# Optimization experiments

Measured on AMD Instinct MI355X. Metric: run time of the kernel, lower is better.

## Reference

```python
import jax, jax.numpy as jnp
import numpy as np

B, N, E, H = 4, 2048, 256, 4
D = E // H  # dim_head = 64


def setup_inputs() -> dict:
    key = jax.random.key(0)
    ks = jax.random.split(key, 8)
    r = lambda k, shape, s=0.02: jax.random.normal(k, shape, jnp.float32) * s
    return dict(
        x0=jax.random.normal(ks[0], (B, N, E), jnp.float32),
        x1=jax.random.normal(ks[1], (B, N, E), jnp.float32),
        Wqk=r(ks[2], (E, E)), bqk=jnp.zeros((E,), jnp.float32),
        Wv=r(ks[3], (E, E)), bv=jnp.zeros((E,), jnp.float32),
        Wo=r(ks[4], (E, E)), bo=jnp.zeros((E,), jnp.float32),
        W1=r(ks[5], (2 * E, 2 * E)), b1=jnp.zeros((2 * E,), jnp.float32),
        g_ln=jnp.ones((2 * E,), jnp.float32), b_ln=jnp.zeros((2 * E,), jnp.float32),
        W2=r(ks[6], (E, 2 * E)), b2=jnp.zeros((E,), jnp.float32),
    )


def _ln(x, g, b, eps=1e-5):
    m = x.mean(-1, keepdims=True)
    v = x.var(-1, keepdims=True)
    return (x - m) * jax.lax.rsqrt(v + eps) * g + b


def reference(x0, x1, Wqk, bqk, Wv, bv, Wo, bo, W1, b1, g_ln, b_ln, W2, b2):
    lin = lambda x, W, b: x @ W.T + b  # torch Linear convention: W is [out, in]
    split = lambda t: t.reshape(B, N, H, D).transpose(0, 2, 1, 3)  # [B,H,N,D]
    merge = lambda t: t.transpose(0, 2, 1, 3).reshape(B, N, E)
    mult = D ** -0.25  # scale**0.5 applied to both qk0 and qk1

    qk0 = split(lin(x0, Wqk, bqk)) * mult
    qk1 = split(lin(x1, Wqk, bqk)) * mult
    v0 = split(lin(x0, Wv, bv))
    v1 = split(lin(x1, Wv, bv))

    sim = jnp.einsum('bhid,bhjd->bhij', qk0, qk1)  # shared similarity [B,H,N0,N1]
    attn01 = jax.nn.softmax(sim, axis=-1)                       # softmax over N1
    attn10 = jax.nn.softmax(jnp.swapaxes(sim, -2, -1), axis=-1)  # [B,H,N1,N0], softmax over N0

    m0 = jnp.einsum('bhij,bhjd->bhid', attn01, v1)  # messages to x0 tokens
    m1 = jnp.einsum('bhij,bhjd->bhid', attn10, v0)  # messages to x1 tokens
    m0 = lin(merge(m0), Wo, bo)
    m1 = lin(merge(m1), Wo, bo)

    def ffn(x, m):
        h = lin(jnp.concatenate([x, m], -1), W1, b1)
        h = jax.nn.gelu(_ln(h, g_ln, b_ln), approximate=False)  # torch GELU = exact erf
        return x + lin(h, W2, b2)

    return (ffn(x0, m0), ffn(x1, m1), attn01, attn10)
```

## Files before the change

kernel.cpp:

```cpp
#include <hip/hip_runtime.h>


typedef unsigned short u16;
typedef unsigned int u32;
typedef __bf16 bf16x8 __attribute__((ext_vector_type(8)));
typedef float f32x4 __attribute__((ext_vector_type(4)));

#define DEV static __device__ __forceinline__

constexpr float MULT2_ = 0.42466090013685146f;

DEV u16 f2bf(float f){ __bf16 h = (__bf16)f; return __builtin_bit_cast(u16, h); }
DEV float bf2f(u16 h){ return __builtin_bit_cast(float, (u32)h << 16); }

DEV f32x4 mfma16(bf16x8 a, bf16x8 b, f32x4 c){
  return __builtin_amdgcn_mfma_f32_16x16x32_bf16(a, b, c, 0, 0, 0);
}

DEV void barrier_ndv(){
  asm volatile("s_waitcnt lgkmcnt(0)" ::: "memory");
  __builtin_amdgcn_s_barrier();
  asm volatile("" ::: "memory");
}

typedef const __attribute__((address_space(1))) void cvoid_g;
typedef __attribute__((address_space(3))) void void_l;
DEV void gload16(const void* g, void* l){
  __builtin_amdgcn_global_load_lds((cvoid_g*)g, (void_l*)l, 16, 0, 0);
}

__global__ __launch_bounds__(256) void cast_k(
    const float* __restrict__ x0, const float* __restrict__ x1,
    const float* __restrict__ Wqk, const float* __restrict__ Wv,
    const float* __restrict__ Wo,  const float* __restrict__ W1,
    const float* __restrict__ W2,
    u16* __restrict__ xc0, u16* __restrict__ xc1,
    u16* __restrict__ Wqkv, u16* __restrict__ WoB,
    u16* __restrict__ W1B,  u16* __restrict__ W2B)
{
  int bid = blockIdx.x;
  if (bid < 1024){
    int s = bid >> 9;
    const float* x = s ? x1 : x0;
    u16* xc = s ? xc1 : xc0;
    for (int v = (bid&511)*256 + threadIdx.x; v < 8192*64; v += 512*256){
      float4 f = ((const float4*)x)[v];
      int m = v >> 6, e4 = (v & 63) << 2;
      ushort4 o;
      o.x = f2bf(f.x); o.y = f2bf(f.y); o.z = f2bf(f.z); o.w = f2bf(f.w);
      *(ushort4*)&xc[(size_t)m*512 + e4] = o;
    }
  } else {
    int t0 = (bid-1024)*256 + threadIdx.x;
    for (int t = t0; t < 512*256; t += 256*256)
      Wqkv[t] = f2bf(t < 65536 ? Wqk[t] : Wv[t - 65536]);
    for (int t = t0; t < 256*256; t += 256*256) WoB[t] = f2bf(Wo[t]);
    for (int t = t0; t < 512*512; t += 256*256) W1B[t] = f2bf(W1[t]);
    for (int t = t0; t < 256*512; t += 256*256) W2B[t] = f2bf(W2[t]);
  }
}

template<int EPI, int K, int LDA, int NT>
__global__ __launch_bounds__(256) void gemm_k(
    const u16* __restrict__ A0, const u16* __restrict__ A1,
    const u16* __restrict__ Bw,
    const float* __restrict__ bias, const float* __restrict__ bias2,
    u16* __restrict__ O0, u16* __restrict__ O1,
    u16* __restrict__ P0, u16* __restrict__ P1,
    const float* __restrict__ R0, const float* __restrict__ R1,
    float* __restrict__ Y)
{
  constexpr int MF = (NT==128) ? 4 : 2;
  __shared__ u16 As[2][128*32];
  __shared__ u16 Bs[2][NT*32];
  const int tid = threadIdx.x, w = tid>>6, l = tid&63;
  const int s = blockIdx.z;
  const u16* A = s ? A1 : A0;
  const int m0 = blockIdx.x*128, n0 = blockIdx.y*NT;
  const int wr = (NT==128) ? (w>>1)*64 : w*32;
  const int wc = (NT==128) ? (w&1)*64 : 0;
  const f32x4 z4 = {0.f,0.f,0.f,0.f};
  f32x4 acc[MF][4];
  #pragma unroll
  for (int i=0;i<MF;++i)
    #pragma unroll
    for (int j=0;j<4;++j) acc[i][j] = z4;
  const int srow = l>>2, sc8 = (l&3)*8;
  auto STAGE = [&](int buf, int kt){
    gload16(&A [(size_t)(m0+w*32   +srow)*LDA + kt + sc8], &As[buf][w*1024]);
    gload16(&A [(size_t)(m0+w*32+16+srow)*LDA + kt + sc8], &As[buf][w*1024+512]);
    if constexpr (NT==128){
      gload16(&Bw[(size_t)(n0+w*32   +srow)*K + kt + sc8], &Bs[buf][w*1024]);
      gload16(&Bw[(size_t)(n0+w*32+16+srow)*K + kt + sc8], &Bs[buf][w*1024+512]);
    } else {
      gload16(&Bw[(size_t)(n0+w*16+srow)*K + kt + sc8], &Bs[buf][w*512]);
    }
  };
  STAGE(0, 0);
  __syncthreads();
  int cur = 0;
  for (int kt = 0; kt < K; kt += 32){
    if (kt+32 < K) STAGE(cur^1, kt+32);
    bf16x8 af[MF], bfr[4];
    #pragma unroll
    for (int mf=0; mf<MF; ++mf)
      af[mf] = *(const bf16x8*)&As[cur][(wr+mf*16+(l&15))*32 + (l>>4)*8];
    #pragma unroll
    for (int nf=0; nf<4; ++nf)
      bfr[nf] = *(const bf16x8*)&Bs[cur][(wc+nf*16+(l&15))*32 + (l>>4)*8];
    #pragma unroll
    for (int mf=0; mf<MF; ++mf)
      #pragma unroll
      for (int nf=0; nf<4; ++nf)
        acc[mf][nf] = mfma16(af[mf], bfr[nf], acc[mf][nf]);
    __syncthreads();
    cur ^= 1;
  }
  u16* Oq = s ? O1 : O0;
  u16* Ov = s ? P1 : P0;
  const float* R = s ? R1 : R0;
  #pragma unroll
  for (int mf=0; mf<MF; ++mf){
    #pragma unroll
    for (int nf=0; nf<4; ++nf){
      #pragma unroll
      for (int r=0; r<4; ++r){
        int row = m0 + wr + mf*16 + (l>>4)*4 + r;
        int col = n0 + wc + nf*16 + (l&15);
        float v = acc[mf][nf][r];
        if constexpr (EPI==0){
          int bb = row >> 11, n = row & 2047;
          if (col < 256){
            float q = (v + bias[col]) * MULT2_;
            int hh = col >> 6, d = col & 63;
            Oq[(size_t)((bb*4+hh)*2048 + n)*64 + d] = f2bf(q);
          } else {
            int c2 = col - 256;
            int hh = c2 >> 6, d = c2 & 63;
            Ov[(size_t)((bb*4+hh)*2048 + n)*64 + d] = f2bf(v + bias2[c2]);
          }
        } else if constexpr (EPI==1){
          Oq[(size_t)row*512 + 256 + col] = f2bf(v + bias[col]);
        } else if constexpr (EPI==2){
          Oq[(size_t)row*512 + col] = f2bf(v + bias[col]);
        } else {
          float* Yp = Y + (size_t)s*2097152;
          Yp[(size_t)row*256 + col] = v + bias[col] + R[(size_t)row*256 + col];
        }
      }
    }
  }
}

__global__ __launch_bounds__(256) void transp_k(
    const u16* __restrict__ v0, const u16* __restrict__ v1,
    u16* __restrict__ t0p, u16* __restrict__ t1p)
{
  __shared__ u16 t[64*66];
  const u16* vin = blockIdx.z ? v1 : v0;
  u16* vout = blockIdx.z ? t1p : t0p;
  int bh = blockIdx.y, j0 = blockIdx.x*64, tid = threadIdx.x;
  #pragma unroll
  for (int r=0;r<2;++r){
    int j = r*32 + (tid>>3), d = (tid&7)*8;
    *(uint4*)&t[j*66 + d] = *(const uint4*)&vin[((size_t)bh*2048 + j0 + j)*64 + d];
  }
  __syncthreads();
  #pragma unroll
  for (int r=0;r<2;++r){
    int d = r*32 + (tid>>3), j8 = (tid&7)*8;
    u32 p[4];
    #pragma unroll
    for (int k=0;k<4;++k){
      u32 lo = t[(j8+2*k)*66 + d];
      u32 hi = t[(j8+2*k+1)*66 + d];
      p[k] = lo | (hi<<16);
    }
    uint4 o = {p[0],p[1],p[2],p[3]};
    *(uint4*)&vout[((size_t)bh*64 + d)*2048 + j0 + j8] = o;
  }
}

__global__ __launch_bounds__(256) void stats2_k(
    const u16* __restrict__ qk0, const u16* __restrict__ qk1,
    float* __restrict__ rps, float* __restrict__ psum)
{
  __shared__ u16 Ks[128*72];
  __shared__ float csumw[4*128];
  int bsw = (int)blockIdx.x;
  int id = (bsw&7)*128 + (bsw>>3);
  const int it = id & 15, jc = (id>>4)&3, bh = id>>6;
  const int i0 = it*128, j0 = jc*512;
  const int tid = threadIdx.x, w = tid>>6, l = tid&63;
  const u16* Qb = qk0 + (size_t)bh*2048*64;
  const u16* Kb = qk1 + (size_t)bh*2048*64;
  bf16x8 qf[2][2];
  #pragma unroll
  for (int mf=0; mf<2; ++mf)
    #pragma unroll
    for (int kf=0; kf<2; ++kf)
      qf[mf][kf] = *(const bf16x8*)&Qb[(size_t)(i0 + w*32 + mf*16 + (l&15))*64 + kf*32 + (l>>4)*8];
  float rlv[2][4];
  #pragma unroll
  for (int mf=0;mf<2;++mf)
    #pragma unroll
    for (int r=0;r<4;++r) rlv[mf][r] = 0.f;
  const int krow = tid>>3, kc = (tid&7)*8;
  uint4 kreg[4];
  #pragma unroll
  for (int r=0;r<4;++r)
    kreg[r] = *(const uint4*)&Kb[(size_t)(j0+r*32+krow)*64 + kc];
  const f32x4 z4 = {0.f,0.f,0.f,0.f};
  for (int jt=j0; jt<j0+512; jt+=128){
    barrier_ndv();
    #pragma unroll
    for (int r=0;r<4;++r) *(uint4*)&Ks[(r*32+krow)*72 + kc] = kreg[r];
    if (jt+128 < j0+512){
      #pragma unroll
      for (int r=0;r<4;++r)
        kreg[r] = *(const uint4*)&Kb[(size_t)(jt+128+r*32+krow)*64 + kc];
    }
    barrier_ndv();
    f32x4 acc[2][8];
    #pragma unroll
    for (int mf=0;mf<2;++mf)
      #pragma unroll
      for (int nf=0;nf<8;++nf) acc[mf][nf] = z4;
    #pragma unroll
    for (int nf=0; nf<8; ++nf){
      bf16x8 b0 = *(const bf16x8*)&Ks[(nf*16+(l&15))*72 + (l>>4)*8];
      bf16x8 b1 = *(const bf16x8*)&Ks[(nf*16+(l&15))*72 + 32 + (l>>4)*8];
      acc[0][nf] = mfma16(qf[0][0], b0, acc[0][nf]);
      acc[0][nf] = mfma16(qf[0][1], b1, acc[0][nf]);
      acc[1][nf] = mfma16(qf[1][0], b0, acc[1][nf]);
      acc[1][nf] = mfma16(qf[1][1], b1, acc[1][nf]);
    }
    #pragma unroll
    for (int mf=0;mf<2;++mf)
      #pragma unroll
      for (int nf=0;nf<8;++nf)
        #pragma unroll
        for (int r=0;r<4;++r)
          acc[mf][nf][r] = exp2f(acc[mf][nf][r]);
    #pragma unroll
    for (int mf=0; mf<2; ++mf)
      #pragma unroll
      for (int r=0; r<4; ++r){
        float ps = 0.f;
        #pragma unroll
        for (int nf=0; nf<8; ++nf) ps += acc[mf][nf][r];
        ps += __shfl_xor(ps, 1);
        ps += __shfl_xor(ps, 2);
        ps += __shfl_xor(ps, 4);
        ps += __shfl_xor(ps, 8);
        rlv[mf][r] += ps;
      }
    float cs[8];
    #pragma unroll
    for (int nf=0; nf<8; ++nf){
      float s = 0.f;
      #pragma unroll
      for (int mf=0;mf<2;++mf)
        #pragma unroll
        for (int r=0;r<4;++r) s += acc[mf][nf][r];
      s += __shfl_xor(s, 16);
      s += __shfl_xor(s, 32);
      cs[nf] = s;
    }
    if (l < 16){
      #pragma unroll
      for (int nf=0; nf<8; ++nf)
        csumw[w*128 + nf*16 + l] = cs[nf];
    }
    barrier_ndv();
    if (tid < 128){
      float s = csumw[tid] + csumw[128+tid] + csumw[256+tid] + csumw[384+tid];
      psum[((size_t)bh*16 + it)*2048 + jt + tid] = s;
    }
  }
  if ((l&15)==0){
    #pragma unroll
    for (int mf=0;mf<2;++mf)
      #pragma unroll
      for (int r=0;r<4;++r){
        int i = i0 + w*32 + mf*16 + (l>>4)*4 + r;
        rps[((size_t)bh*4 + jc)*2048 + i] = rlv[mf][r];
      }
  }
}

__global__ __launch_bounds__(256) void reduce_k(
    const float* __restrict__ rps, const float* __restrict__ psum,
    float* __restrict__ c0, float* __restrict__ c1)
{
  int idx = blockIdx.x*256 + threadIdx.x;
  int bh = idx >> 11, i = idx & 2047;
  if (blockIdx.y == 0){
    float s = 0.f;
    #pragma unroll
    for (int c=0;c<4;++c) s += rps[((size_t)bh*4 + c)*2048 + i];
    c0[bh*2048 + i] = log2f(s);
  } else {
    float s = 0.f;
    #pragma unroll
    for (int it=0; it<16; ++it) s += psum[((size_t)bh*16 + it)*2048 + i];
    c1[bh*2048 + i] = log2f(s);
  }
}

__global__ __launch_bounds__(256) void attn_k(
    const u16* __restrict__ qk0, const u16* __restrict__ qk1,
    const u16* __restrict__ vT0, const u16* __restrict__ vT1,
    const float* __restrict__ c0, const float* __restrict__ c1,
    u16* __restrict__ mo0, u16* __restrict__ mo1,
    float* __restrict__ dout)
{
  __shared__ u16 Ks[128*72];
  __shared__ u16 Vs[64*136];
  __shared__ u16 Ps[128*136];
  int bsw = (int)blockIdx.x;
  int id = (bsw&7)*64 + (bsw>>3);
  const int it = id & 15, bh = (id>>4)&15, z = id>>8;
  const u16* Q  = z ? qk1 : qk0;
  const u16* Kp = z ? qk0 : qk1;
  const u16* Vp = z ? vT0 : vT1;
  const float* cc = z ? c1 : c0;
  u16* mo = z ? mo1 : mo0;
  const int i0 = it*128;
  float* aout = dout + (size_t)(z ? 71303168u : 4194304u) + (size_t)bh*4194304u;
  const int tid = threadIdx.x, w = tid>>6, l = tid&63;
  const u16* Qb = Q + (size_t)bh*2048*64;
  const u16* Kb = Kp + (size_t)bh*2048*64;
  const u16* Vb = Vp + (size_t)bh*64*2048;
  bf16x8 qf[8][2];
  #pragma unroll
  for (int nf=0; nf<8; ++nf)
    #pragma unroll
    for (int kf=0; kf<2; ++kf)
      qf[nf][kf] = *(const bf16x8*)&Qb[(size_t)(i0 + nf*16 + (l&15))*64 + kf*32 + (l>>4)*8];
  float rci[8];
  #pragma unroll
  for (int nf=0;nf<8;++nf)
    rci[nf] = cc[bh*2048 + i0 + nf*16 + (l&15)];
  const f32x4 z4 = {0.f,0.f,0.f,0.f};
  f32x4 macc[2][4];
  #pragma unroll
  for (int mf=0;mf<2;++mf)
    #pragma unroll
    for (int nf=0;nf<4;++nf) macc[mf][nf] = z4;
  const int krow = tid>>3, kc = (tid&7)*8;
  const int vd = tid>>4, vc = (tid&15)*8;
  uint4 kreg[4], vreg[4];
  #pragma unroll
  for (int r=0;r<4;++r){
    kreg[r] = *(const uint4*)&Kb[(size_t)(r*32+krow)*64 + kc];
    vreg[r] = *(const uint4*)&Vb[(size_t)(r*16+vd)*2048 + vc];
  }
  for (int jt=0; jt<2048; jt+=128){
    barrier_ndv();
    #pragma unroll
    for (int r=0;r<4;++r) *(uint4*)&Ks[(r*32+krow)*72 + kc] = kreg[r];
    #pragma unroll
    for (int r=0;r<4;++r) *(uint4*)&Vs[(r*16+vd)*136 + vc] = vreg[r];
    if (jt+128 < 2048){
      #pragma unroll
      for (int r=0;r<4;++r){
        kreg[r] = *(const uint4*)&Kb[(size_t)(jt+128+r*32+krow)*64 + kc];
        vreg[r] = *(const uint4*)&Vb[(size_t)(r*16+vd)*2048 + jt+128 + vc];
      }
    }
    barrier_ndv();
    f32x4 acc[2][8];
    #pragma unroll
    for (int mf=0;mf<2;++mf)
      #pragma unroll
      for (int nf=0;nf<8;++nf) acc[mf][nf] = z4;
    #pragma unroll
    for (int mf=0; mf<2; ++mf){
      bf16x8 a0 = *(const bf16x8*)&Ks[(w*32+mf*16+(l&15))*72 + (l>>4)*8];
      bf16x8 a1 = *(const bf16x8*)&Ks[(w*32+mf*16+(l&15))*72 + 32 + (l>>4)*8];
      #pragma unroll
      for (int nf=0; nf<8; ++nf){
        acc[mf][nf] = mfma16(a0, qf[nf][0], acc[mf][nf]);
        acc[mf][nf] = mfma16(a1, qf[nf][1], acc[mf][nf]);
      }
    }
    #pragma unroll
    for (int mf=0;mf<2;++mf){
      int jlb = w*32 + mf*16 + (l>>4)*4;
      #pragma unroll
      for (int nf=0;nf<8;++nf){
        int i = nf*16 + (l&15);
        f32x4 pv;
        #pragma unroll
        for (int r=0;r<4;++r) pv[r] = exp2f(acc[mf][nf][r]-rci[nf]);
        __builtin_nontemporal_store(pv,
            (f32x4*)&aout[(size_t)(i0+i)*2048 + jt + jlb]);
        u16 pb[4];
        #pragma unroll
        for (int r=0;r<4;++r) pb[r] = f2bf(pv[r]);
        u32 w0 = (u32)pb[0] | ((u32)pb[1]<<16);
        u32 w1 = (u32)pb[2] | ((u32)pb[3]<<16);
        uint2 pk = {w0, w1};
        *(uint2*)&Ps[i*136 + jlb] = pk;
      }
    }
    barrier_ndv();
    #pragma unroll
    for (int kf=0; kf<4; ++kf){
      bf16x8 pa0 = *(const bf16x8*)&Ps[(w*32 + (l&15))*136 + kf*32 + (l>>4)*8];
      bf16x8 pa1 = *(const bf16x8*)&Ps[(w*32 + 16 + (l&15))*136 + kf*32 + (l>>4)*8];
      #pragma unroll
      for (int nf=0; nf<4; ++nf){
        bf16x8 vb = *(const bf16x8*)&Vs[(nf*16+(l&15))*136 + kf*32 + (l>>4)*8];
        macc[0][nf] = mfma16(pa0, vb, macc[0][nf]);
        macc[1][nf] = mfma16(pa1, vb, macc[1][nf]);
      }
    }
  }
  int bb = bh>>2, hh = bh&3;
  #pragma unroll
  for (int mf=0;mf<2;++mf)
    #pragma unroll
    for (int nf=0;nf<4;++nf)
      #pragma unroll
      for (int r=0;r<4;++r){
        int n = i0 + w*32 + mf*16 + (l>>4)*4 + r;
        int d = nf*16 + (l&15);
        mo[(size_t)(bb*2048 + n)*256 + hh*64 + d] = f2bf(macc[mf][nf][r]);
      }
}

__global__ __launch_bounds__(256) void ln_gelu_k(
    u16* __restrict__ h0, u16* __restrict__ h1,
    const float* __restrict__ g, const float* __restrict__ be)
{
  u16* h = blockIdx.y ? h1 : h0;
  int row = blockIdx.x*4 + (threadIdx.x>>6);
  int l = threadIdx.x & 63;
  u16* hr = h + (size_t)row*512;
  uint4 raw = *(const uint4*)&hr[l*8];
  u32 ua[4] = {raw.x, raw.y, raw.z, raw.w};
  float f[8];
  #pragma unroll
  for (int k=0;k<4;++k){
    f[2*k]   = bf2f((u16)(ua[k] & 0xFFFFu));
    f[2*k+1] = bf2f((u16)(ua[k] >> 16));
  }
  float s = 0.f, s2 = 0.f;
  #pragma unroll
  for (int k=0;k<8;++k){ s += f[k]; s2 += f[k]*f[k]; }
  #pragma unroll
  for (int o=1;o<64;o<<=1){ s += __shfl_xor(s,o); s2 += __shfl_xor(s2,o); }
  float mean = s * (1.f/512.f);
  float var  = s2 * (1.f/512.f) - mean*mean;
  float rstd = rsqrtf(var + 1e-5f);
  u32 ob[4];
  #pragma unroll
  for (int k=0;k<8;++k){
    int e = l*8 + k;
    float t = (f[k]-mean)*rstd*g[e] + be[e];
    float gl = 0.5f*t*(1.f + erff(t*0.70710678118654752f));
    u16 b = f2bf(gl);
    if (k&1) ob[k>>1] |= (u32)b << 16; else ob[k>>1] = (u32)b;
  }
  uint4 o4 = {ob[0],ob[1],ob[2],ob[3]};
  *(uint4*)&hr[l*8] = o4;
}

extern "C" void kernel_launch(void* const* d_in, const int* in_sizes, int n_in,
                              void* d_out, int out_size, void* d_ws, size_t ws_size,
                              hipStream_t stream)
{
  const float* x0  = (const float*)d_in[0];
  const float* x1  = (const float*)d_in[1];
  const float* Wqk = (const float*)d_in[2];
  const float* bqk = (const float*)d_in[3];
  const float* Wv  = (const float*)d_in[4];
  const float* bv  = (const float*)d_in[5];
  const float* Wo  = (const float*)d_in[6];
  const float* bo  = (const float*)d_in[7];
  const float* W1  = (const float*)d_in[8];
  const float* b1  = (const float*)d_in[9];
  const float* gln = (const float*)d_in[10];
  const float* bln = (const float*)d_in[11];
  const float* W2  = (const float*)d_in[12];
  const float* b2  = (const float*)d_in[13];
  (void)in_sizes; (void)n_in; (void)out_size; (void)ws_size;
  float* out = (float*)d_out;
  char* ws = (char*)d_ws;
  size_t off = 0;
  auto alloc = [&](size_t bytes)->void*{
    void* p = ws + off; off += (bytes + 255) & ~(size_t)255; return p; };
  u16* xc0 = (u16*)alloc((size_t)8192*512*2);
  u16* xc1 = (u16*)alloc((size_t)8192*512*2);
  u16* Wqkv= (u16*)alloc((size_t)512*256*2);
  u16* WoB = (u16*)alloc((size_t)256*256*2);
  u16* W1B = (u16*)alloc((size_t)512*512*2);
  u16* W2B = (u16*)alloc((size_t)256*512*2);
  u16* qk0 = (u16*)alloc((size_t)16*2048*64*2);
  u16* qk1 = (u16*)alloc((size_t)16*2048*64*2);
  u16* v0  = (u16*)alloc((size_t)16*2048*64*2);
  u16* v1  = (u16*)alloc((size_t)16*2048*64*2);
  u16* vT0 = (u16*)alloc((size_t)16*2048*64*2);
  u16* vT1 = (u16*)alloc((size_t)16*2048*64*2);
  u16* m0  = (u16*)alloc((size_t)8192*256*2);
  u16* m1  = (u16*)alloc((size_t)8192*256*2);
  u16* h0  = (u16*)alloc((size_t)8192*512*2);
  u16* h1  = (u16*)alloc((size_t)8192*512*2);
  float* c0 = (float*)alloc((size_t)16*2048*4);
  float* c1 = (float*)alloc((size_t)16*2048*4);
  float* psum = (float*)alloc((size_t)16*16*2048*4);
  float* rps  = (float*)alloc((size_t)16*4*2048*4);

  cast_k<<<dim3(1280), 256, 0, stream>>>(x0, x1, Wqk, Wv, Wo, W1, W2,
      xc0, xc1, Wqkv, WoB, W1B, W2B);
  gemm_k<0,256,512,128><<<dim3(64,4,2), 256, 0, stream>>>(
      xc0, xc1, Wqkv, bqk, bv, qk0, qk1, v0, v1, nullptr, nullptr, nullptr);
  transp_k<<<dim3(32,16,2), 256, 0, stream>>>(v0, v1, vT0, vT1);
  stats2_k<<<dim3(1024), 256, 0, stream>>>(qk0, qk1, rps, psum);
  reduce_k<<<dim3(128,2), 256, 0, stream>>>(rps, psum, c0, c1);
  attn_k<<<dim3(512), 256, 0, stream>>>(
      qk0, qk1, vT0, vT1, c0, c1, m0, m1, out);
  gemm_k<1,256,256,64><<<dim3(64,4,2), 256, 0, stream>>>(
      m0, m1, WoB, bo, nullptr, xc0, xc1, nullptr, nullptr, nullptr, nullptr, nullptr);
  gemm_k<2,512,512,128><<<dim3(64,4,2), 256, 0, stream>>>(
      xc0, xc1, W1B, b1, nullptr, h0, h1, nullptr, nullptr, nullptr, nullptr, nullptr);
  ln_gelu_k<<<dim3(2048,2), 256, 0, stream>>>(h0, h1, gln, bln);
  gemm_k<3,512,512,64><<<dim3(64,4,2), 256, 0, stream>>>(
      h0, h1, W2B, b2, nullptr, nullptr, nullptr, nullptr, nullptr, x0, x1, out);
}
```

Measured before the change: 313.3 us.

## Halve attention query tile, load K fragments directly to registers, raise occupancy

```diff
diff --git a/kernel.cpp b/kernel.cpp
--- a/kernel.cpp
+++ b/kernel.cpp
@@ -308,88 +308,88 @@
   }
 }
 
-__global__ __launch_bounds__(256) void attn_k(
+__global__ __launch_bounds__(256, 3) void attn_k(
     const u16* __restrict__ qk0, const u16* __restrict__ qk1,
     const u16* __restrict__ vT0, const u16* __restrict__ vT1,
     const float* __restrict__ c0, const float* __restrict__ c1,
     u16* __restrict__ mo0, u16* __restrict__ mo1,
     float* __restrict__ dout)
 {
-  __shared__ u16 Ks[128*72];
   __shared__ u16 Vs[64*136];
-  __shared__ u16 Ps[128*136];
+  __shared__ u16 Ps[64*136];
   int bsw = (int)blockIdx.x;
-  int id = (bsw&7)*64 + (bsw>>3);
-  const int it = id & 15, bh = (id>>4)&15, z = id>>8;
+  int id = (bsw&7)*128 + (bsw>>3);
+  const int it = id & 31, bh = (id>>5)&15, z = id>>9;
   const u16* Q  = z ? qk1 : qk0;
   const u16* Kp = z ? qk0 : qk1;
   const u16* Vp = z ? vT0 : vT1;
   const float* cc = z ? c1 : c0;
   u16* mo = z ? mo1 : mo0;
-  const int i0 = it*128;
+  const int i0 = it*64;
   float* aout = dout + (size_t)(z ? 71303168u : 4194304u) + (size_t)bh*4194304u;
   const int tid = threadIdx.x, w = tid>>6, l = tid&63;
   const u16* Qb = Q + (size_t)bh*2048*64;
   const u16* Kb = Kp + (size_t)bh*2048*64;
   const u16* Vb = Vp + (size_t)bh*64*2048;
-  bf16x8 qf[8][2];
-  #pragma unroll
-  for (int nf=0; nf<8; ++nf)
+  bf16x8 qf[4][2];
+  #pragma unroll
+  for (int nf=0; nf<4; ++nf)
     #pragma unroll
     for (int kf=0; kf<2; ++kf)
       qf[nf][kf] = *(const bf16x8*)&Qb[(size_t)(i0 + nf*16 + (l&15))*64 + kf*32 + (l>>4)*8];
-  float rci[8];
-  #pragma unroll
-  for (int nf=0;nf<8;++nf)
+  float rci[4];
+  #pragma unroll
+  for (int nf=0;nf<4;++nf)
     rci[nf] = cc[bh*2048 + i0 + nf*16 + (l&15)];
   const f32x4 z4 = {0.f,0.f,0.f,0.f};
-  f32x4 macc[2][4];
+  f32x4 macc[4];
+  #pragma unroll
+  for (int nf=0;nf<4;++nf) macc[nf] = z4;
+  const int kr0 = w*32 + (l&15);
+  bf16x8 ka[2][2], kaN[2][2];
   #pragma unroll
   for (int mf=0;mf<2;++mf)
     #pragma unroll
-    for (int nf=0;nf<4;++nf) macc[mf][nf] = z4;
-  const int krow = tid>>3, kc = (tid&7)*8;
+    for (int h=0;h<2;++h)
+      ka[mf][h] = *(const bf16x8*)&Kb[(size_t)(kr0 + mf*16)*64 + h*32 + (l>>4)*8];
   const int vd = tid>>4, vc = (tid&15)*8;
-  uint4 kreg[4], vreg[4];
-  #pragma unroll
-  for (int r=0;r<4;++r){
-    kreg[r] = *(const uint4*)&Kb[(size_t)(r*32+krow)*64 + kc];
+  uint4 vreg[4];
+  #pragma unroll
+  for (int r=0;r<4;++r)
     vreg[r] = *(const uint4*)&Vb[(size_t)(r*16+vd)*2048 + vc];
-  }
   for (int jt=0; jt<2048; jt+=128){
+    f32x4 acc[2][4];
+    #pragma unroll
+    for (int mf=0;mf<2;++mf)
+      #pragma unroll
+      for (int nf=0;nf<4;++nf) acc[mf][nf] = z4;
+    #pragma unroll
+    for (int mf=0; mf<2; ++mf)
+      #pragma unroll
+      for (int nf=0; nf<4; ++nf){
+        acc[mf][nf] = mfma16(ka[mf][0], qf[nf][0], acc[mf][nf]);
+        acc[mf][nf] = mfma16(ka[mf][1], qf[nf][1], acc[mf][nf]);
+      }
+    if (jt+128 < 2048){
+      #pragma unroll
+      for (int mf=0;mf<2;++mf)
+        #pragma unroll
+        for (int h=0;h<2;++h)
+          kaN[mf][h] = *(const bf16x8*)&Kb[(size_t)(jt+128 + kr0 + mf*16)*64 + h*32 + (l>>4)*8];
+    }
     barrier_ndv();
-    #pragma unroll
-    for (int r=0;r<4;++r) *(uint4*)&Ks[(r*32+krow)*72 + kc] = kreg[r];
     #pragma unroll
     for (int r=0;r<4;++r) *(uint4*)&Vs[(r*16+vd)*136 + vc] = vreg[r];
     if (jt+128 < 2048){
       #pragma unroll
-      for (int r=0;r<4;++r){
-        kreg[r] = *(const uint4*)&Kb[(size_t)(jt+128+r*32+krow)*64 + kc];
+      for (int r=0;r<4;++r)
         vreg[r] = *(const uint4*)&Vb[(size_t)(r*16+vd)*2048 + jt+128 + vc];
-      }
-    }
-    barrier_ndv();
-    f32x4 acc[2][8];
-    #pragma unroll
-    for (int mf=0;mf<2;++mf)
-      #pragma unroll
-      for (int nf=0;nf<8;++nf) acc[mf][nf] = z4;
-    #pragma unroll
-    for (int mf=0; mf<2; ++mf){
-      bf16x8 a0 = *(const bf16x8*)&Ks[(w*32+mf*16+(l&15))*72 + (l>>4)*8];
-      bf16x8 a1 = *(const bf16x8*)&Ks[(w*32+mf*16+(l&15))*72 + 32 + (l>>4)*8];
-      #pragma unroll
-      for (int nf=0; nf<8; ++nf){
-        acc[mf][nf] = mfma16(a0, qf[nf][0], acc[mf][nf]);
-        acc[mf][nf] = mfma16(a1, qf[nf][1], acc[mf][nf]);
-      }
     }
     #pragma unroll
     for (int mf=0;mf<2;++mf){
       int jlb = w*32 + mf*16 + (l>>4)*4;
       #pragma unroll
-      for (int nf=0;nf<8;++nf){
+      for (int nf=0;nf<4;++nf){
         int i = nf*16 + (l&15);
         f32x4 pv;
         #pragma unroll
@@ -408,27 +408,28 @@
     barrier_ndv();
     #pragma unroll
     for (int kf=0; kf<4; ++kf){
-      bf16x8 pa0 = *(const bf16x8*)&Ps[(w*32 + (l&15))*136 + kf*32 + (l>>4)*8];
-      bf16x8 pa1 = *(const bf16x8*)&Ps[(w*32 + 16 + (l&15))*136 + kf*32 + (l>>4)*8];
+      bf16x8 pa = *(const bf16x8*)&Ps[(w*16 + (l&15))*136 + kf*32 + (l>>4)*8];
       #pragma unroll
       for (int nf=0; nf<4; ++nf){
         bf16x8 vb = *(const bf16x8*)&Vs[(nf*16+(l&15))*136 + kf*32 + (l>>4)*8];
-        macc[0][nf] = mfma16(pa0, vb, macc[0][nf]);
-        macc[1][nf] = mfma16(pa1, vb, macc[1][nf]);
+        macc[nf] = mfma16(pa, vb, macc[nf]);
       }
     }
+    #pragma unroll
+    for (int mf=0;mf<2;++mf)
+      #pragma unroll
+      for (int h=0;h<2;++h)
+        ka[mf][h] = kaN[mf][h];
   }
   int bb = bh>>2, hh = bh&3;
   #pragma unroll
-  for (int mf=0;mf<2;++mf)
-    #pragma unroll
-    for (int nf=0;nf<4;++nf)
-      #pragma unroll
-      for (int r=0;r<4;++r){
-        int n = i0 + w*32 + mf*16 + (l>>4)*4 + r;
-        int d = nf*16 + (l&15);
-        mo[(size_t)(bb*2048 + n)*256 + hh*64 + d] = f2bf(macc[mf][nf][r]);
-      }
+  for (int nf=0;nf<4;++nf)
+    #pragma unroll
+    for (int r=0;r<4;++r){
+      int n = i0 + w*16 + (l>>4)*4 + r;
+      int d = nf*16 + (l&15);
+      mo[(size_t)(bb*2048 + n)*256 + hh*64 + d] = f2bf(macc[nf][r]);
+    }
 }
 
 __global__ __launch_bounds__(256) void ln_gelu_k(
@@ -520,7 +521,7 @@
   transp_k<<<dim3(32,16,2), 256, 0, stream>>>(v0, v1, vT0, vT1);
   stats2_k<<<dim3(1024), 256, 0, stream>>>(qk0, qk1, rps, psum);
   reduce_k<<<dim3(128,2), 256, 0, stream>>>(rps, psum, c0, c1);
-  attn_k<<<dim3(512), 256, 0, stream>>>(
+  attn_k<<<dim3(1024), 256, 0, stream>>>(
       qk0, qk1, vT0, vT1, c0, c1, m0, m1, out);
   gemm_k<1,256,256,64><<<dim3(64,4,2), 256, 0, stream>>>(
       m0, m1, WoB, bo, nullptr, xc0, xc1, nullptr, nullptr, nullptr, nullptr, nullptr);
```

Measured after the change: 314.4 us. Within noise of the previous version (+0.3%).
